# Performance work log

Hardware: AMD Instinct MI355X
Metric: run time of the kernel (lower is better)

Reference implementation:

```python
import jax, jax.numpy as jnp
import numpy as np

N_NODES = 50000
N_EDGES = 1200000
BATCH = 64
D_IN = 2
D_EMB = 64
EPS = 1e-12


def _l2norm(x):
    # torch.nn.functional.normalize(dim=1): x / max(||x||_2, eps)
    n = jnp.sqrt(jnp.sum(x * x, axis=1, keepdims=True))
    return x / jnp.maximum(n, EPS)


def setup_inputs() -> dict:
    key = jax.random.key(0)
    ks = jax.random.split(key, 10)
    edge_row = jnp.sort(jax.random.randint(ks[0], (N_EDGES,), 0, N_NODES, dtype=jnp.int32))
    edge_col = jax.random.randint(ks[1], (N_EDGES,), 0, N_NODES, dtype=jnp.int32)
    batch_assign = jax.random.randint(ks[2], (N_NODES,), 0, BATCH, dtype=jnp.int32)
    input_features = jax.random.uniform(ks[3], (N_NODES, D_IN), dtype=jnp.float32)
    input_feature_s = jax.random.uniform(ks[4], (BATCH, D_IN), dtype=jnp.float32)
    W1 = jax.random.normal(ks[5], (D_IN, D_EMB), dtype=jnp.float32) * 0.1
    W2 = jax.random.normal(ks[6], (D_EMB, D_EMB), dtype=jnp.float32) * 0.1
    W3 = jax.random.normal(ks[7], (D_EMB, D_EMB), dtype=jnp.float32) * 0.1
    Wl = jax.random.normal(ks[8], (2 * D_EMB, D_EMB), dtype=jnp.float32) * 0.1
    bl = jnp.zeros((D_EMB,), dtype=jnp.float32)
    return {
        "edge_row": edge_row, "edge_col": edge_col, "batch_assign": batch_assign,
        "input_features": input_features, "input_feature_s": input_feature_s,
        "W1": W1, "W2": W2, "W3": W3, "Wl": Wl, "bl": bl, "depth": 3,
    }


def reference(edge_row, edge_col, batch_assign, input_features, input_feature_s,
              W1, W2, W3, Wl, bl, depth):
    n_nodes = input_features.shape[0]
    n_batch = input_feature_s.shape[0]

    h = _l2norm(jax.nn.relu(input_features @ W1))        # [N, d]
    hs = _l2norm(jax.nn.relu(input_feature_s @ W1))      # [B, d]

    for _ in range(depth):
        # SPMM node_node @ h : gather neighbor embeddings, sum per destination row
        h_nv = jax.ops.segment_sum(h[edge_col], edge_row, num_segments=n_nodes)  # [N, d]
        # SPMM batch_node @ h : pool node embeddings per graph
        h_nv_s = jax.ops.segment_sum(h, batch_assign, num_segments=n_batch)      # [B, d]
        h = _l2norm(jax.nn.relu(jnp.concatenate([h @ W2, h_nv @ W3], axis=1) @ Wl + bl))
        hs = _l2norm(jax.nn.relu(jnp.concatenate([hs @ W2, h_nv_s @ W3], axis=1) @ Wl + bl))
    return (h, hs)
```

## Files before the change

### kernel.cpp

```cpp
#include <hip/hip_runtime.h>
#include <math.h>

#define N_NODES 50000
#define N_EDGES 1200000
#define BATCH   64
#define D       64
#define EPS     1e-12f
#define NCOPY   64

__global__ void k_rowstart(const int* __restrict__ edge_row, int* __restrict__ row_start,
                           float* __restrict__ pools ) {
    int tid = blockIdx.x * blockDim.x + threadIdx.x;
    int nthr = gridDim.x * blockDim.x;
    for (int i = tid; i < 2 * NCOPY * BATCH * D; i += nthr) pools[i] = 0.f;
    if (tid > N_NODES) return;
    int lo = 0, hi = N_EDGES;
    while (lo < hi) {
        int mid = (lo + hi) >> 1;
        if (edge_row[mid] < tid) lo = mid + 1; else hi = mid;
    }
    row_start[tid] = lo;
}

__global__ void k_fuse(const float* __restrict__ W2, const float* __restrict__ W3,
                       const float* __restrict__ Wl, float* __restrict__ MM) {
    int k = blockIdx.x, j = threadIdx.x;
    float a2 = 0.f, a3 = 0.f;
    for (int t = 0; t < D; ++t) {
        a2 += W2[k*D + t] * Wl[t*D + j];
        a3 += W3[k*D + t] * Wl[(D + t)*D + j];
    }
    MM[k*2*D + 2*j]     = a2;
    MM[k*2*D + 2*j + 1] = a3;
}

__device__ __forceinline__ float lane_bcast(float v, int k) {
    return __uint_as_float(__builtin_amdgcn_readlane(__float_as_uint(v), k));
}

__device__ __forceinline__ float wave_l2norm(float v) {
    float ss = v * v;
    #pragma unroll
    for (int off = 32; off; off >>= 1) ss += __shfl_xor(ss, off);
    return sqrtf(ss);
}

__global__ void __launch_bounds__(256) k_init(const float* __restrict__ X,
                                              const float* __restrict__ Xs,
                                              const float* __restrict__ W1,
                                              float* __restrict__ B0,
                                              float* __restrict__ HS,
                                              const int* __restrict__ batch,
                                              float* __restrict__ P0) {
    int row = blockIdx.x * 4 + (threadIdx.x >> 6);
    int j   = threadIdx.x & 63;
    if (row >= N_NODES + BATCH) return;
    float x0, x1; float* out;
    bool is_node = (row < N_NODES);
    if (is_node) {
        x0 = X[row*2]; x1 = X[row*2 + 1]; out = B0 + (size_t)row * D;
    } else {
        int r = row - N_NODES;
        x0 = Xs[r*2]; x1 = Xs[r*2 + 1]; out = HS + (size_t)r * D;
    }
    float v = fmaxf(fmaf(x0, W1[j], x1 * W1[D + j]), 0.f);
    float n = wave_l2norm(v);
    float val = v / fmaxf(n, EPS);
    out[j] = val;
    if (is_node) {
        int b = __builtin_amdgcn_readfirstlane(batch[row]);
        atomicAdd(&P0[(blockIdx.x & (NCOPY - 1)) * (BATCH * D) + b * D + j], val);
    }
}

__global__ void __launch_bounds__(512, 4) k_iter(const int* __restrict__ edge_col,
                                                 const int* __restrict__ row_start,
                                                 const float* __restrict__ Hc,
                                                 float* __restrict__ Hn,
                                                 const float* __restrict__ MM,
                                                 const float* __restrict__ bl,
                                                 const int* __restrict__ batch,
                                                 float* __restrict__ Pout) {
    __shared__ float sMM[2 * D * D];
    int t = threadIdx.x;
    for (int i = t; i < 2 * D * D; i += 512) sMM[i] = MM[i];
    __syncthreads();
    int row = blockIdx.x * 8 + (t >> 6);
    int l = t & 63;

    int s = __builtin_amdgcn_readfirstlane(row_start[row]);
    int e = __builtin_amdgcn_readfirstlane(row_start[row + 1]);

    float hv = Hc[(size_t)row * D + l];
    const float* __restrict__ Hl = Hc + l;

    float acc = 0.f;
    int pad = 0;
    for (int base = s; base < e; base += 64) {
        int cw = e - base; if (cw > 64) cw = 64;
        int col = 0;
        if (l < cw) col = edge_col[base + l];
        int nb = (cw + 15) >> 4;
        pad += (nb << 4) - cw;
        for (int b = 0; b < nb; ++b) {
            int o = b << 4;
            #pragma unroll
            for (int u = 0; u < 16; ++u) {
                int c = __builtin_amdgcn_readlane(col, o + u);
                acc += Hl[(size_t)c * D];
            }
        }
    }
    acc -= (float)pad * Hl[0];
    float gv = acc;

    float a2 = 0.f, a3 = bl[l];
    #pragma unroll
    for (int k = 0; k < D; ++k) {
        float hk = lane_bcast(hv, k);
        float gk = lane_bcast(gv, k);
        float2 mm = *(const float2*)&sMM[k * 2 * D + 2 * l];
        a2 = fmaf(hk, mm.x, a2);
        a3 = fmaf(gk, mm.y, a3);
    }
    float v = fmaxf(a2 + a3, 0.f);
    float n = wave_l2norm(v);
    float val = v / fmaxf(n, EPS);
    Hn[(size_t)row * D + l] = val;

    if (Pout) {
        int b = __builtin_amdgcn_readfirstlane(batch[row]);
        atomicAdd(&Pout[(blockIdx.x & (NCOPY - 1)) * (BATCH * D) + b * D + l], val);
    }
}

__global__ void __launch_bounds__(256) k_hs(float* __restrict__ HS,
                                            float* __restrict__ P,
                                            const float* __restrict__ MM,
                                            const float* __restrict__ bl) {
    __shared__ float sMM[2 * D * D];
    int t = threadIdx.x;
    for (int i = t; i < 2 * D * D; i += 256) sMM[i] = MM[i];
    __syncthreads();
    int row = blockIdx.x * 4 + (t >> 6);
    int j = t & 63;
    float* base = P + row * D + j;
    float g0 = 0.f, g1 = 0.f, g2 = 0.f, g3 = 0.f;
    #pragma unroll 8
    for (int c = 0; c < NCOPY; c += 4) {
        float v0 = base[(size_t)(c + 0) * (BATCH * D)];
        float v1 = base[(size_t)(c + 1) * (BATCH * D)];
        float v2 = base[(size_t)(c + 2) * (BATCH * D)];
        float v3 = base[(size_t)(c + 3) * (BATCH * D)];
        base[(size_t)(c + 0) * (BATCH * D)] = 0.f;
        base[(size_t)(c + 1) * (BATCH * D)] = 0.f;
        base[(size_t)(c + 2) * (BATCH * D)] = 0.f;
        base[(size_t)(c + 3) * (BATCH * D)] = 0.f;
        g0 += v0; g1 += v1; g2 += v2; g3 += v3;
    }
    float gv = (g0 + g1) + (g2 + g3);
    float hv = HS[(size_t)row * D + j];
    float a2 = 0.f, a3 = bl[j];
    #pragma unroll
    for (int k = 0; k < D; ++k) {
        float hk = lane_bcast(hv, k);
        float gk = lane_bcast(gv, k);
        float2 mm = *(const float2*)&sMM[k * 2 * D + 2 * j];
        a2 = fmaf(hk, mm.x, a2);
        a3 = fmaf(gk, mm.y, a3);
    }
    float v = fmaxf(a2 + a3, 0.f);
    float n = wave_l2norm(v);
    HS[(size_t)row * D + j] = v / fmaxf(n, EPS);
}

extern "C" void kernel_launch(void* const* d_in, const int* in_sizes, int n_in,
                              void* d_out, int out_size, void* d_ws, size_t ws_size,
                              hipStream_t stream) {
    const int*   edge_row = (const int*)  d_in[0];
    const int*   edge_col = (const int*)  d_in[1];
    const int*   batch    = (const int*)  d_in[2];
    const float* X        = (const float*)d_in[3];
    const float* Xs       = (const float*)d_in[4];
    const float* W1       = (const float*)d_in[5];
    const float* W2       = (const float*)d_in[6];
    const float* W3       = (const float*)d_in[7];
    const float* Wl       = (const float*)d_in[8];
    const float* bl       = (const float*)d_in[9];

    float* H  = (float*)d_out;
    float* HS = (float*)d_out + (size_t)N_NODES * D;

    float* B0  = (float*)d_ws;
    float* B1  = B0 + (size_t)N_NODES * D;
    float* PA  = B1 + (size_t)N_NODES * D;
    float* PB  = PA + (size_t)NCOPY * BATCH * D;
    float* MM  = PB + (size_t)NCOPY * BATCH * D;
    int*   row_start = (int*)(MM + 2 * D * D);

    const int nblk = N_NODES / 8;

    k_rowstart<<<(N_NODES + 256) / 256, 256, 0, stream>>>(edge_row, row_start, PA);
    k_fuse<<<D, D, 0, stream>>>(W2, W3, Wl, MM);
    k_init<<<(N_NODES + BATCH + 3) / 4, 256, 0, stream>>>(X, Xs, W1, B0, HS, batch, PA);

    k_iter<<<nblk, 512, 0, stream>>>(edge_col, row_start, B0, B1, MM, bl, batch, PB);
    k_hs<<<16, 256, 0, stream>>>(HS, PA, MM, bl);

    k_iter<<<nblk, 512, 0, stream>>>(edge_col, row_start, B1, B0, MM, bl, batch, PA);
    k_hs<<<16, 256, 0, stream>>>(HS, PB, MM, bl);

    k_iter<<<nblk, 512, 0, stream>>>(edge_col, row_start, B0, H, MM, bl, batch, nullptr);
    k_hs<<<16, 256, 0, stream>>>(HS, PA, MM, bl);
}
```

Baseline: 301.8 us.

## Fuse batch-pool update into node iteration kernel, process two rows per wave

Merges row_start/zeroing and weight-fusion kernels into one prep launch, and folds the per-graph pooled update into extra blocks of the node iteration kernel, removing three k_hs launches and one prep launch. Each wave now handles two consecutive rows, walking their combined edge range once, and the dense 64x128 matmul is done from shared-memory broadcast of packed h/g values with a float4-interleaved weight layout, so each weight load serves two rows. Occupancy hint rises to 8 blocks per CU. Risks: branchy per-edge accumulation into A or B, extra shared memory, and register pressure from the higher launch bound.

```diff
diff --git a/kernel.cpp b/kernel.cpp
--- a/kernel.cpp
+++ b/kernel.cpp
@@ -7,42 +7,48 @@
 #define D       64
 #define EPS     1e-12f
 #define NCOPY   64
-
-__global__ void k_rowstart(const int* __restrict__ edge_row, int* __restrict__ row_start,
-                           float* __restrict__ pools ) {
-    int tid = blockIdx.x * blockDim.x + threadIdx.x;
-    int nthr = gridDim.x * blockDim.x;
-    for (int i = tid; i < 2 * NCOPY * BATCH * D; i += nthr) pools[i] = 0.f;
-    if (tid > N_NODES) return;
-    int lo = 0, hi = N_EDGES;
-    while (lo < hi) {
-        int mid = (lo + hi) >> 1;
-        if (edge_row[mid] < tid) lo = mid + 1; else hi = mid;
-    }
-    row_start[tid] = lo;
-}
-
-__global__ void k_fuse(const float* __restrict__ W2, const float* __restrict__ W3,
-                       const float* __restrict__ Wl, float* __restrict__ MM) {
-    int k = blockIdx.x, j = threadIdx.x;
-    float a2 = 0.f, a3 = 0.f;
-    for (int t = 0; t < D; ++t) {
-        a2 += W2[k*D + t] * Wl[t*D + j];
-        a3 += W3[k*D + t] * Wl[(D + t)*D + j];
-    }
-    MM[k*2*D + 2*j]     = a2;
-    MM[k*2*D + 2*j + 1] = a3;
-}
-
-__device__ __forceinline__ float lane_bcast(float v, int k) {
-    return __uint_as_float(__builtin_amdgcn_readlane(__float_as_uint(v), k));
+#define NODE_BLOCKS 3125
+#define HS_BLOCKS   4
+#define ITER_GRID  (NODE_BLOCKS + HS_BLOCKS)
+
+__device__ __forceinline__ int rfl(int v) { return __builtin_amdgcn_readfirstlane(v); }
+
+__global__ void __launch_bounds__(512) k_prep(const int* __restrict__ edge_row,
+                                              int* __restrict__ row_start,
+                                              float* __restrict__ pools,
+                                              const float* __restrict__ W2,
+                                              const float* __restrict__ W3,
+                                              const float* __restrict__ Wl,
+                                              float* __restrict__ MM4) {
+    if (blockIdx.x < 98) {
+        int tid = blockIdx.x * 512 + threadIdx.x;
+        for (int i = tid; i < 2 * NCOPY * BATCH * D; i += 98 * 512) pools[i] = 0.f;
+        if (tid > N_NODES) return;
+        int lo = 0, hi = N_EDGES;
+        while (lo < hi) {
+            int mid = (lo + hi) >> 1;
+            if (edge_row[mid] < tid) lo = mid + 1; else hi = mid;
+        }
+        row_start[tid] = lo;
+    } else {
+        for (int p = threadIdx.x; p < D * D; p += 512) {
+            int k = p >> 6, j = p & 63;
+            float a2 = 0.f, a3 = 0.f;
+            for (int q = 0; q < D; ++q) {
+                a2 += W2[k*D + q] * Wl[q*D + j];
+                a3 += W3[k*D + q] * Wl[(D + q)*D + j];
+            }
+            MM4[(k >> 1) * D * 4 + j * 4 + (k & 1) * 2 + 0] = a2;
+            MM4[(k >> 1) * D * 4 + j * 4 + (k & 1) * 2 + 1] = a3;
+        }
+    }
 }
 
 __device__ __forceinline__ float wave_l2norm(float v) {
     float ss = v * v;
     #pragma unroll
     for (int off = 32; off; off >>= 1) ss += __shfl_xor(ss, off);
-    return sqrtf(ss);
+    return ss;
 }
 
 __global__ void __launch_bounds__(256) k_init(const float* __restrict__ X,
@@ -64,114 +70,121 @@
         x0 = Xs[r*2]; x1 = Xs[r*2 + 1]; out = HS + (size_t)r * D;
     }
     float v = fmaxf(fmaf(x0, W1[j], x1 * W1[D + j]), 0.f);
-    float n = wave_l2norm(v);
+    float n = sqrtf(wave_l2norm(v));
     float val = v / fmaxf(n, EPS);
     out[j] = val;
     if (is_node) {
-        int b = __builtin_amdgcn_readfirstlane(batch[row]);
+        int b = rfl(batch[row]);
         atomicAdd(&P0[(blockIdx.x & (NCOPY - 1)) * (BATCH * D) + b * D + j], val);
     }
 }
 
-__global__ void __launch_bounds__(512, 4) k_iter(const int* __restrict__ edge_col,
+__global__ void __launch_bounds__(512, 8) k_iter(const int* __restrict__ edge_col,
                                                  const int* __restrict__ row_start,
                                                  const float* __restrict__ Hc,
                                                  float* __restrict__ Hn,
-                                                 const float* __restrict__ MM,
+                                                 const float* __restrict__ MM4,
                                                  const float* __restrict__ bl,
                                                  const int* __restrict__ batch,
-                                                 float* __restrict__ Pout) {
-    __shared__ float sMM[2 * D * D];
+                                                 float* __restrict__ Pout,
+                                                 float* __restrict__ HSrw,
+                                                 float* __restrict__ Pin) {
+    __shared__ float4 sMM[32 * 64];
+    __shared__ float4 sHG[8 * 64];
     int t = threadIdx.x;
-    for (int i = t; i < 2 * D * D; i += 512) sMM[i] = MM[i];
+    const float4* gMM = (const float4*)MM4;
+    for (int i = t; i < 32 * 64; i += 512) sMM[i] = gMM[i];
     __syncthreads();
-    int row = blockIdx.x * 8 + (t >> 6);
-    int l = t & 63;
-
-    int s = __builtin_amdgcn_readfirstlane(row_start[row]);
-    int e = __builtin_amdgcn_readfirstlane(row_start[row + 1]);
-
-    float hv = Hc[(size_t)row * D + l];
-    const float* __restrict__ Hl = Hc + l;
-
-    float acc = 0.f;
-    int pad = 0;
-    for (int base = s; base < e; base += 64) {
-        int cw = e - base; if (cw > 64) cw = 64;
-        int col = 0;
-        if (l < cw) col = edge_col[base + l];
-        int nb = (cw + 15) >> 4;
-        pad += (nb << 4) - cw;
-        for (int b = 0; b < nb; ++b) {
-            int o = b << 4;
-            #pragma unroll
-            for (int u = 0; u < 16; ++u) {
-                int c = __builtin_amdgcn_readlane(col, o + u);
-                acc += Hl[(size_t)c * D];
+    int w = t >> 6, l = t & 63;
+    bool is_node = (blockIdx.x < NODE_BLOCKS);
+    int rA, rB;
+    float hvA, hvB, gvA, gvB;
+
+    if (is_node) {
+        int pr = blockIdx.x * 8 + w;
+        rA = 2 * pr; rB = rA + 1;
+        int sA = rfl(row_start[rA]);
+        int eA = rfl(row_start[rB]);
+        int eB = rfl(row_start[rB + 1]);
+        hvA = Hc[(size_t)rA * D + l];
+        hvB = Hc[(size_t)rB * D + l];
+        float aA = 0.f, aB = 0.f;
+        int pad = 0;
+        for (int base = sA; base < eB; ) {
+            int cw = eB - base; if (cw > 64) cw = 64;
+            int col = 0;
+            if (l < cw) col = edge_col[base + l];
+            int nb = (cw + 15) >> 4;
+            pad += (nb << 4) - cw;
+            for (int b = 0; b < nb; ++b) {
+                #pragma unroll
+                for (int u = 0; u < 16; ++u) {
+                    int idx = (b << 4) + u;
+                    int c = __builtin_amdgcn_readlane(col, idx);
+                    const float* rp = Hc + (size_t)c * D;
+                    float v = rp[l];
+                    if (base + idx < eA) aA += v; else aB += v;
+                }
             }
-        }
-    }
-    acc -= (float)pad * Hl[0];
-    float gv = acc;
-
-    float a2 = 0.f, a3 = bl[l];
+            base += cw;
+        }
+        aB -= (float)pad * Hc[l];
+        gvA = aA; gvB = aB;
+    } else {
+        int pr = (blockIdx.x - NODE_BLOCKS) * 8 + w;
+        rA = 2 * pr; rB = rA + 1;
+        hvA = HSrw[(size_t)rA * D + l];
+        hvB = HSrw[(size_t)rB * D + l];
+        float aA = 0.f, aB = 0.f;
+        #pragma unroll 4
+        for (int c = 0; c < NCOPY; ++c) {
+            float* pA = Pin + (size_t)c * (BATCH * D) + rA * D + l;
+            float vA = pA[0], vB = pA[D];
+            pA[0] = 0.f; pA[D] = 0.f;
+            aA += vA; aB += vB;
+        }
+        gvA = aA; gvB = aB;
+    }
+
+    sHG[w * 64 + l] = make_float4(hvA, hvB, gvA, gvB);
+    float biasl = bl[l];
+    float a2x = 0.f, a2y = 0.f, a3x = biasl, a3y = biasl;
+    const float4* hg = &sHG[w * 64];
     #pragma unroll
-    for (int k = 0; k < D; ++k) {
-        float hk = lane_bcast(hv, k);
-        float gk = lane_bcast(gv, k);
-        float2 mm = *(const float2*)&sMM[k * 2 * D + 2 * l];
-        a2 = fmaf(hk, mm.x, a2);
-        a3 = fmaf(gk, mm.y, a3);
-    }
-    float v = fmaxf(a2 + a3, 0.f);
-    float n = wave_l2norm(v);
-    float val = v / fmaxf(n, EPS);
-    Hn[(size_t)row * D + l] = val;
-
-    if (Pout) {
-        int b = __builtin_amdgcn_readfirstlane(batch[row]);
-        atomicAdd(&Pout[(blockIdx.x & (NCOPY - 1)) * (BATCH * D) + b * D + l], val);
-    }
-}
-
-__global__ void __launch_bounds__(256) k_hs(float* __restrict__ HS,
-                                            float* __restrict__ P,
-                                            const float* __restrict__ MM,
-                                            const float* __restrict__ bl) {
-    __shared__ float sMM[2 * D * D];
-    int t = threadIdx.x;
-    for (int i = t; i < 2 * D * D; i += 256) sMM[i] = MM[i];
-    __syncthreads();
-    int row = blockIdx.x * 4 + (t >> 6);
-    int j = t & 63;
-    float* base = P + row * D + j;
-    float g0 = 0.f, g1 = 0.f, g2 = 0.f, g3 = 0.f;
-    #pragma unroll 8
-    for (int c = 0; c < NCOPY; c += 4) {
-        float v0 = base[(size_t)(c + 0) * (BATCH * D)];
-        float v1 = base[(size_t)(c + 1) * (BATCH * D)];
-        float v2 = base[(size_t)(c + 2) * (BATCH * D)];
-        float v3 = base[(size_t)(c + 3) * (BATCH * D)];
-        base[(size_t)(c + 0) * (BATCH * D)] = 0.f;
-        base[(size_t)(c + 1) * (BATCH * D)] = 0.f;
-        base[(size_t)(c + 2) * (BATCH * D)] = 0.f;
-        base[(size_t)(c + 3) * (BATCH * D)] = 0.f;
-        g0 += v0; g1 += v1; g2 += v2; g3 += v3;
-    }
-    float gv = (g0 + g1) + (g2 + g3);
-    float hv = HS[(size_t)row * D + j];
-    float a2 = 0.f, a3 = bl[j];
+    for (int kk = 0; kk < 32; ++kk) {
+        float4 mm = sMM[kk * 64 + l];
+        float4 h0 = hg[2 * kk];
+        float4 h1 = hg[2 * kk + 1];
+        a2x = fmaf(h0.x, mm.x, a2x); a2y = fmaf(h0.y, mm.x, a2y);
+        a3x = fmaf(h0.z, mm.y, a3x); a3y = fmaf(h0.w, mm.y, a3y);
+        a2x = fmaf(h1.x, mm.z, a2x); a2y = fmaf(h1.y, mm.z, a2y);
+        a3x = fmaf(h1.z, mm.w, a3x); a3y = fmaf(h1.w, mm.w, a3y);
+    }
+    float vA = fmaxf(a2x + a3x, 0.f);
+    float vB = fmaxf(a2y + a3y, 0.f);
+    float ssA = vA * vA, ssB = vB * vB;
     #pragma unroll
-    for (int k = 0; k < D; ++k) {
-        float hk = lane_bcast(hv, k);
-        float gk = lane_bcast(gv, k);
-        float2 mm = *(const float2*)&sMM[k * 2 * D + 2 * j];
-        a2 = fmaf(hk, mm.x, a2);
-        a3 = fmaf(gk, mm.y, a3);
-    }
-    float v = fmaxf(a2 + a3, 0.f);
-    float n = wave_l2norm(v);
-    HS[(size_t)row * D + j] = v / fmaxf(n, EPS);
+    for (int off = 32; off; off >>= 1) {
+        ssA += __shfl_xor(ssA, off);
+        ssB += __shfl_xor(ssB, off);
+    }
+    float oA = vA / fmaxf(sqrtf(ssA), EPS);
+    float oB = vB / fmaxf(sqrtf(ssB), EPS);
+
+    if (is_node) {
+        Hn[(size_t)rA * D + l] = oA;
+        Hn[(size_t)rB * D + l] = oB;
+        if (Pout) {
+            int bA = rfl(batch[rA]);
+            int bB = rfl(batch[rB]);
+            float* cp = Pout + (size_t)(blockIdx.x & (NCOPY - 1)) * (BATCH * D);
+            atomicAdd(&cp[bA * D + l], oA);
+            atomicAdd(&cp[bB * D + l], oB);
+        }
+    } else {
+        HSrw[(size_t)rA * D + l] = oA;
+        HSrw[(size_t)rB * D + l] = oB;
+    }
 }
 
 extern "C" void kernel_launch(void* const* d_in, const int* in_sizes, int n_in,
@@ -195,21 +208,13 @@
     float* B1  = B0 + (size_t)N_NODES * D;
     float* PA  = B1 + (size_t)N_NODES * D;
     float* PB  = PA + (size_t)NCOPY * BATCH * D;
-    float* MM  = PB + (size_t)NCOPY * BATCH * D;
-    int*   row_start = (int*)(MM + 2 * D * D);
-
-    const int nblk = N_NODES / 8;
-
-    k_rowstart<<<(N_NODES + 256) / 256, 256, 0, stream>>>(edge_row, row_start, PA);
-    k_fuse<<<D, D, 0, stream>>>(W2, W3, Wl, MM);
+    float* MM4 = PB + (size_t)NCOPY * BATCH * D;
+    int*   row_start = (int*)(MM4 + 32 * 64 * 4);
+
+    k_prep<<<99, 512, 0, stream>>>(edge_row, row_start, PA, W2, W3, Wl, MM4);
     k_init<<<(N_NODES + BATCH + 3) / 4, 256, 0, stream>>>(X, Xs, W1, B0, HS, batch, PA);
 
-    k_iter<<<nblk, 512, 0, stream>>>(edge_col, row_start, B0, B1, MM, bl, batch, PB);
-    k_hs<<<16, 256, 0, stream>>>(HS, PA, MM, bl);
-
-    k_iter<<<nblk, 512, 0, stream>>>(edge_col, row_start, B1, B0, MM, bl, batch, PA);
-    k_hs<<<16, 256, 0, stream>>>(HS, PB, MM, bl);
-
-    k_iter<<<nblk, 512, 0, stream>>>(edge_col, row_start, B0, H, MM, bl, batch, nullptr);
-    k_hs<<<16, 256, 0, stream>>>(HS, PA, MM, bl);
-}
+    k_iter<<<ITER_GRID, 512, 0, stream>>>(edge_col, row_start, B0, B1, MM4, bl, batch, PB, HS, PA);
+    k_iter<<<ITER_GRID, 512, 0, stream>>>(edge_col, row_start, B1, B0, MM4, bl, batch, PA, HS, PB);
+    k_iter<<<ITER_GRID, 512, 0, stream>>>(edge_col, row_start, B0, H, MM4, bl, batch, nullptr, HS, PA);
+}
```

After: 281.7 us. 1.07x faster.
